# Kernel tuning notes

Measured on AMD Instinct MI355X. Metric: run time of the kernel, lower is better.

Reference implementation:

```python
import jax, jax.numpy as jnp
import numpy as np

B, T, D = 16, 4096, 1024
NUM_CLASSES = 1000
K, TOP_M = 4, 8
TEMP, EPS = 0.07, 1e-6


def setup_inputs() -> dict:
    key = jax.random.key(0)
    k_e, k_v, k_w = jax.random.split(key, 3)
    E = jax.random.normal(k_e, (B, T, D), dtype=jnp.float32)
    v = jax.random.normal(k_v, (K, D), dtype=jnp.float32) * 0.02
    m_logits = jnp.zeros((K, D), dtype=jnp.float32)
    cls_W = jax.random.normal(k_w, (K, NUM_CLASSES, D), dtype=jnp.float32) * (1.0 / D ** 0.5)
    cls_b = jnp.zeros((K, NUM_CLASSES), dtype=jnp.float32)
    beta = jnp.ones((K,), dtype=jnp.float32)
    alpha = jnp.ones((K,), dtype=jnp.float32)
    return {"E": E, "v": v, "m_logits": m_logits, "cls_W": cls_W,
            "cls_b": cls_b, "beta": beta, "alpha": alpha}


def reference(E, v, m_logits, cls_W, cls_b, beta, alpha):
    tokens = E  # (B, T, D)
    logits_sum = jnp.zeros((E.shape[0], cls_W.shape[1]), dtype=E.dtype)
    top_m = min(TOP_M, E.shape[1])
    for k in range(K):
        # unit peel direction u_k
        vk = v[k] * jax.nn.sigmoid(m_logits[k])          # (D,)
        u = vk / (jnp.linalg.norm(vk) + EPS)             # (D,)
        # token scores and soft attention
        coeff_all = jnp.einsum('btd,d->bt', tokens, u)   # (B, T) = E @ u
        scores = coeff_all / TEMP
        att = jax.nn.softmax(scores, axis=1)             # (B, T)
        # hard top-m tokens
        _, top_idx = jax.lax.top_k(scores, top_m)        # (B, m)
        top_tokens = jnp.take_along_axis(tokens, top_idx[:, :, None], axis=1)  # (B, m, D)
        # rank-1 projections onto u: proj(X) = (X@u)[...,None]*u
        coeff_top = jnp.einsum('bmd,d->bm', top_tokens, u)
        z_hard = jnp.sum(coeff_top, axis=1)[:, None] * u           # (B, D)
        z_soft = jnp.sum(coeff_all * att, axis=1)[:, None] * u     # (B, D)
        z_k = 0.5 * (z_hard + z_soft)
        logits_k = z_k @ cls_W[k].T + cls_b[k]                      # (B, C)
        logits_sum = logits_sum + alpha[k] * logits_k
        # residual peel: remove u component from all tokens
        tokens = tokens - beta[k] * (coeff_all[:, :, None] * u)
    return logits_sum
```

## Files before the change

kernel.cpp:

```cpp
#include <hip/hip_runtime.h>
#include <math.h>

#define DD 1024
#define TT 4096
#define BB 16
#define KK 4
#define CC 1000
#define TEMP_F 0.07f
#define EPS_F 1e-6f
#define NPROJ 2048

#define CE(a, b) { float _mx = fmaxf(a, b), _mn = fminf(a, b); a = _mx; b = _mn; }
#define INS8(y_) { float y = (y_); \
    CE(s0, y) CE(s1, y) CE(s2, y) CE(s3, y) CE(s4, y) CE(s5, y) CE(s6, y) CE(s7, y) }
#define RESORT8() { \
    CE(s0, s4) CE(s1, s5) CE(s2, s6) CE(s3, s7) \
    CE(s0, s2) CE(s1, s3) CE(s4, s6) CE(s5, s7) \
    CE(s0, s1) CE(s2, s3) CE(s4, s5) CE(s6, s7) }
#define WMERGE(off) { \
    float t0 = __shfl_xor(s0, off), t1 = __shfl_xor(s1, off), \
          t2 = __shfl_xor(s2, off), t3 = __shfl_xor(s3, off), \
          t4 = __shfl_xor(s4, off), t5 = __shfl_xor(s5, off), \
          t6 = __shfl_xor(s6, off), t7 = __shfl_xor(s7, off); \
    s0 = fmaxf(s0, t7); s1 = fmaxf(s1, t6); s2 = fmaxf(s2, t5); s3 = fmaxf(s3, t4); \
    s4 = fmaxf(s4, t3); s5 = fmaxf(s5, t2); s6 = fmaxf(s6, t1); s7 = fmaxf(s7, t0); \
    RESORT8() }
#define LMERGE(L) { \
    s0 = fmaxf(s0, (L)[7]); s1 = fmaxf(s1, (L)[6]); s2 = fmaxf(s2, (L)[5]); \
    s3 = fmaxf(s3, (L)[4]); s4 = fmaxf(s4, (L)[3]); s5 = fmaxf(s5, (L)[2]); \
    s6 = fmaxf(s6, (L)[1]); s7 = fmaxf(s7, (L)[0]); \
    RESORT8() }

__global__ __launch_bounds__(256) void k_u_g(const float* __restrict__ v,
                                             const float* __restrict__ m,
                                             float* __restrict__ u_ws,
                                             float* __restrict__ G_ws) {
    __shared__ float u_lds[KK * DD];
    int tid = threadIdx.x, w = tid >> 6, lane = tid & 63;
    float s_reg[16];
    float ss = 0.f;
#pragma unroll
    for (int i = 0; i < 16; ++i) {
        int d = lane + i * 64;
        float mv = m[w * DD + d];
        float s = v[w * DD + d] * (1.f / (1.f + expf(-mv)));
        s_reg[i] = s; ss += s * s;
    }
#pragma unroll
    for (int off = 32; off; off >>= 1) ss += __shfl_xor(ss, off);
    float inv = 1.f / (sqrtf(ss) + EPS_F);
#pragma unroll
    for (int i = 0; i < 16; ++i) {
        int d = lane + i * 64;
        float uu = s_reg[i] * inv;
        u_lds[w * DD + d] = uu;
        u_ws[w * DD + d] = uu;
    }
    __syncthreads();
    for (int p = w; p < 6; p += 4) {
        int j = (p < 3) ? 0 : ((p < 5) ? 1 : 2);
        int k = (p < 3) ? (p + 1) : ((p < 5) ? (p - 1) : 3);
        float acc = 0.f;
#pragma unroll
        for (int i = 0; i < 16; ++i) {
            int d = lane + i * 64;
            acc += u_lds[j * DD + d] * u_lds[k * DD + d];
        }
#pragma unroll
        for (int off = 32; off; off >>= 1) acc += __shfl_xor(acc, off);
        if (lane == 0) G_ws[j * KK + k] = acc;
    }
}

__global__ __launch_bounds__(256) void k_proj_wu(const float* __restrict__ E,
                                                 const float* __restrict__ W,
                                                 const float* __restrict__ u_ws,
                                                 float* __restrict__ c0,
                                                 float* __restrict__ wdot) {
    int tid = threadIdx.x, w = tid >> 6, lane = tid & 63;
    if (blockIdx.x < NPROJ) {
        float4 U[KK][4];
#pragma unroll
        for (int k = 0; k < KK; ++k)
#pragma unroll
            for (int j = 0; j < 4; ++j)
                U[k][j] = *reinterpret_cast<const float4*>(u_ws + k * DD + lane * 4 + j * 256);
        const int ITERS = (BB * TT) / (NPROJ * 4);
#pragma unroll 1
        for (int it = 0; it < ITERS; ++it) {
            size_t g = (size_t)(blockIdx.x * 4 + w) + (size_t)it * (NPROJ * 4);
            const float* e = E + g * DD;
            float a0 = 0.f, a1 = 0.f, a2 = 0.f, a3 = 0.f;
#pragma unroll
            for (int j = 0; j < 4; ++j) {
                float4 ev = *reinterpret_cast<const float4*>(e + lane * 4 + j * 256);
                a0 += ev.x * U[0][j].x + ev.y * U[0][j].y + ev.z * U[0][j].z + ev.w * U[0][j].w;
                a1 += ev.x * U[1][j].x + ev.y * U[1][j].y + ev.z * U[1][j].z + ev.w * U[1][j].w;
                a2 += ev.x * U[2][j].x + ev.y * U[2][j].y + ev.z * U[2][j].z + ev.w * U[2][j].w;
                a3 += ev.x * U[3][j].x + ev.y * U[3][j].y + ev.z * U[3][j].z + ev.w * U[3][j].w;
            }
#pragma unroll
            for (int off = 32; off; off >>= 1) {
                a0 += __shfl_xor(a0, off);
                a1 += __shfl_xor(a1, off);
                a2 += __shfl_xor(a2, off);
                a3 += __shfl_xor(a3, off);
            }
            if (lane == 0)
                *reinterpret_cast<float4*>(c0 + g * 4) = make_float4(a0, a1, a2, a3);
        }
    } else {
        int c = blockIdx.x - NPROJ;
        const float* wr = W + ((size_t)w * CC + c) * DD;
        const float* ur = u_ws + w * DD;
        float acc = 0.f;
#pragma unroll
        for (int j = 0; j < 4; ++j) {
            float4 wv = *reinterpret_cast<const float4*>(wr + lane * 4 + j * 256);
            float4 uv = *reinterpret_cast<const float4*>(ur + lane * 4 + j * 256);
            acc += wv.x * uv.x + wv.y * uv.y + wv.z * uv.z + wv.w * uv.w;
        }
#pragma unroll
        for (int off = 32; off; off >>= 1) acc += __shfl_xor(acc, off);
        if (lane == 0) wdot[w * CC + c] = acc;
    }
}

__global__ __launch_bounds__(256) void k_peel2(const float* __restrict__ c0,
                                               const float* __restrict__ G_ws,
                                               const float* __restrict__ beta,
                                               float* __restrict__ cscal) {
    __shared__ float redm[4], reds[4], redc[4];
    __shared__ float topl[4][8];
    int tid = threadIdx.x, w = tid >> 6, lane = tid & 63;
    int b = blockIdx.x >> 2, k = blockIdx.x & 3;
    float g01 = G_ws[0 * KK + 1], g02 = G_ws[0 * KK + 2], g03 = G_ws[0 * KK + 3];
    float g12 = G_ws[1 * KK + 2], g13 = G_ws[1 * KK + 3], g23 = G_ws[2 * KK + 3];
    float b0 = beta[0], b1 = beta[1], b2 = beta[2];
    float fk[16];
    float mx = -INFINITY;
#pragma unroll
    for (int i = 0; i < 16; ++i) {
        int t = tid + i * 256;
        float4 cv = *reinterpret_cast<const float4*>(c0 + ((size_t)b * TT + t) * 4);
        float f0 = cv.x;
        float f1 = cv.y - b0 * g01 * f0;
        float f2 = cv.z - b0 * g02 * f0 - b1 * g12 * f1;
        float f3 = cv.w - b0 * g03 * f0 - b1 * g13 * f1 - b2 * g23 * f2;
        float f = (k == 0) ? f0 : ((k == 1) ? f1 : ((k == 2) ? f2 : f3));
        fk[i] = f; mx = fmaxf(mx, f);
    }
#pragma unroll
    for (int off = 32; off; off >>= 1) mx = fmaxf(mx, __shfl_xor(mx, off));
    if (lane == 0) redm[w] = mx;
    __syncthreads();
    mx = fmaxf(fmaxf(redm[0], redm[1]), fmaxf(redm[2], redm[3]));
    const float invT = 1.f / TEMP_F;
    float se = 0.f, sce = 0.f;
#pragma unroll
    for (int i = 0; i < 16; ++i) {
        float e = expf((fk[i] - mx) * invT);
        se += e; sce += fk[i] * e;
    }
#pragma unroll
    for (int off = 32; off; off >>= 1) {
        se += __shfl_xor(se, off);
        sce += __shfl_xor(sce, off);
    }
    if (lane == 0) { reds[w] = se; redc[w] = sce; }
    __syncthreads();
    se = reds[0] + reds[1] + reds[2] + reds[3];
    sce = redc[0] + redc[1] + redc[2] + redc[3];
    float zsoft = sce / se;
    float s0 = -INFINITY, s1 = -INFINITY, s2 = -INFINITY, s3 = -INFINITY,
          s4 = -INFINITY, s5 = -INFINITY, s6 = -INFINITY, s7 = -INFINITY;
#pragma unroll
    for (int i = 0; i < 16; ++i) INS8(fk[i]);
    WMERGE(1) WMERGE(2) WMERGE(4) WMERGE(8) WMERGE(16) WMERGE(32)
    if (lane == 0) {
        topl[w][0] = s0; topl[w][1] = s1; topl[w][2] = s2; topl[w][3] = s3;
        topl[w][4] = s4; topl[w][5] = s5; topl[w][6] = s6; topl[w][7] = s7;
    }
    __syncthreads();
    if (tid == 0) {
        LMERGE(topl[1]) LMERGE(topl[2]) LMERGE(topl[3])
        float sumtop = s0 + s1 + s2 + s3 + s4 + s5 + s6 + s7;
        cscal[b * KK + k] = 0.5f * (sumtop + zsoft);
    }
}

__global__ __launch_bounds__(256) void k_out(const float* __restrict__ wdot,
                                             const float* __restrict__ bias,
                                             const float* __restrict__ alpha,
                                             const float* __restrict__ cscal,
                                             float* __restrict__ out) {
    int idx = blockIdx.x * 256 + threadIdx.x;
    if (idx >= BB * CC) return;
    int b = idx / CC, c = idx % CC;
    float s = 0.f;
#pragma unroll
    for (int k = 0; k < KK; ++k)
        s += alpha[k] * (cscal[b * KK + k] * wdot[k * CC + c] + bias[k * CC + c]);
    out[idx] = s;
}

extern "C" void kernel_launch(void* const* d_in, const int* in_sizes, int n_in,
                              void* d_out, int out_size, void* d_ws, size_t ws_size,
                              hipStream_t stream) {
    const float* E     = (const float*)d_in[0];
    const float* v     = (const float*)d_in[1];
    const float* m     = (const float*)d_in[2];
    const float* W     = (const float*)d_in[3];
    const float* cb    = (const float*)d_in[4];
    const float* beta  = (const float*)d_in[5];
    const float* alpha = (const float*)d_in[6];
    float* out = (float*)d_out;
    float* ws = (float*)d_ws;

    float* u_ws  = ws;
    float* G_ws  = ws + 4096;
    float* cscal = ws + 4112;
    float* wdot  = ws + 4176;
    float* c0    = ws + 8176;

    k_u_g<<<1, 256, 0, stream>>>(v, m, u_ws, G_ws);
    k_proj_wu<<<NPROJ + CC, 256, 0, stream>>>(E, W, u_ws, c0, wdot);
    k_peel2<<<BB * KK, 256, 0, stream>>>(c0, G_ws, beta, cscal);
    k_out<<<(BB * CC + 255) / 256, 256, 0, stream>>>(wdot, cb, alpha, cscal, out);
}
```

Baseline: 64.87 us.

## Fuse u/Gram setup into projection kernel and peel into output kernel

After: 72.13 us. 1.11x slower.

```diff
diff --git a/kernel.cpp b/kernel.cpp
--- a/kernel.cpp
+++ b/kernel.cpp
@@ -25,36 +25,33 @@
     s0 = fmaxf(s0, t7); s1 = fmaxf(s1, t6); s2 = fmaxf(s2, t5); s3 = fmaxf(s3, t4); \
     s4 = fmaxf(s4, t3); s5 = fmaxf(s5, t2); s6 = fmaxf(s6, t1); s7 = fmaxf(s7, t0); \
     RESORT8() }
-#define LMERGE(L) { \
-    s0 = fmaxf(s0, (L)[7]); s1 = fmaxf(s1, (L)[6]); s2 = fmaxf(s2, (L)[5]); \
-    s3 = fmaxf(s3, (L)[4]); s4 = fmaxf(s4, (L)[3]); s5 = fmaxf(s5, (L)[2]); \
-    s6 = fmaxf(s6, (L)[1]); s7 = fmaxf(s7, (L)[0]); \
-    RESORT8() }
 
-__global__ __launch_bounds__(256) void k_u_g(const float* __restrict__ v,
-                                             const float* __restrict__ m,
-                                             float* __restrict__ u_ws,
-                                             float* __restrict__ G_ws) {
+__global__ __launch_bounds__(256) void k_main(const float* __restrict__ E,
+                                              const float* __restrict__ W,
+                                              const float* __restrict__ v,
+                                              const float* __restrict__ m,
+                                              const float* __restrict__ beta,
+                                              float* __restrict__ c0,
+                                              float* __restrict__ wdot) {
     __shared__ float u_lds[KK * DD];
+    __shared__ float G_lds[6];
     int tid = threadIdx.x, w = tid >> 6, lane = tid & 63;
-    float s_reg[16];
-    float ss = 0.f;
+
+    {
+        float s_reg[16];
+        float ss = 0.f;
 #pragma unroll
-    for (int i = 0; i < 16; ++i) {
-        int d = lane + i * 64;
-        float mv = m[w * DD + d];
-        float s = v[w * DD + d] * (1.f / (1.f + expf(-mv)));
-        s_reg[i] = s; ss += s * s;
-    }
+        for (int i = 0; i < 16; ++i) {
+            int d = lane + i * 64;
+            float mv = m[w * DD + d];
+            float s = v[w * DD + d] * (1.f / (1.f + expf(-mv)));
+            s_reg[i] = s; ss += s * s;
+        }
 #pragma unroll
-    for (int off = 32; off; off >>= 1) ss += __shfl_xor(ss, off);
-    float inv = 1.f / (sqrtf(ss) + EPS_F);
+        for (int off = 32; off; off >>= 1) ss += __shfl_xor(ss, off);
+        float inv = 1.f / (sqrtf(ss) + EPS_F);
 #pragma unroll
-    for (int i = 0; i < 16; ++i) {
-        int d = lane + i * 64;
-        float uu = s_reg[i] * inv;
-        u_lds[w * DD + d] = uu;
-        u_ws[w * DD + d] = uu;
+        for (int i = 0; i < 16; ++i) u_lds[w * DD + lane + i * 64] = s_reg[i] * inv;
     }
     __syncthreads();
     for (int p = w; p < 6; p += 4) {
@@ -68,23 +65,20 @@
         }
 #pragma unroll
         for (int off = 32; off; off >>= 1) acc += __shfl_xor(acc, off);
-        if (lane == 0) G_ws[j * KK + k] = acc;
+        if (lane == 0) G_lds[p] = acc;
     }
-}
+    __syncthreads();
 
-__global__ __launch_bounds__(256) void k_proj_wu(const float* __restrict__ E,
-                                                 const float* __restrict__ W,
-                                                 const float* __restrict__ u_ws,
-                                                 float* __restrict__ c0,
-                                                 float* __restrict__ wdot) {
-    int tid = threadIdx.x, w = tid >> 6, lane = tid & 63;
     if (blockIdx.x < NPROJ) {
+        float g01 = G_lds[0], g02 = G_lds[1], g03 = G_lds[2];
+        float g12 = G_lds[3], g13 = G_lds[4], g23 = G_lds[5];
+        float b0 = beta[0], b1 = beta[1], b2 = beta[2];
         float4 U[KK][4];
 #pragma unroll
         for (int k = 0; k < KK; ++k)
 #pragma unroll
             for (int j = 0; j < 4; ++j)
-                U[k][j] = *reinterpret_cast<const float4*>(u_ws + k * DD + lane * 4 + j * 256);
+                U[k][j] = *reinterpret_cast<const float4*>(u_lds + k * DD + lane * 4 + j * 256);
         const int ITERS = (BB * TT) / (NPROJ * 4);
 #pragma unroll 1
         for (int it = 0; it < ITERS; ++it) {
@@ -106,18 +100,21 @@
                 a2 += __shfl_xor(a2, off);
                 a3 += __shfl_xor(a3, off);
             }
+            float f0 = a0;
+            float f1 = a1 - b0 * g01 * f0;
+            float f2 = a2 - b0 * g02 * f0 - b1 * g12 * f1;
+            float f3 = a3 - b0 * g03 * f0 - b1 * g13 * f1 - b2 * g23 * f2;
             if (lane == 0)
-                *reinterpret_cast<float4*>(c0 + g * 4) = make_float4(a0, a1, a2, a3);
+                *reinterpret_cast<float4*>(c0 + g * 4) = make_float4(f0, f1, f2, f3);
         }
     } else {
         int c = blockIdx.x - NPROJ;
         const float* wr = W + ((size_t)w * CC + c) * DD;
-        const float* ur = u_ws + w * DD;
         float acc = 0.f;
 #pragma unroll
         for (int j = 0; j < 4; ++j) {
             float4 wv = *reinterpret_cast<const float4*>(wr + lane * 4 + j * 256);
-            float4 uv = *reinterpret_cast<const float4*>(ur + lane * 4 + j * 256);
+            float4 uv = *reinterpret_cast<const float4*>(u_lds + w * DD + lane * 4 + j * 256);
             acc += wv.x * uv.x + wv.y * uv.y + wv.z * uv.z + wv.w * uv.w;
         }
 #pragma unroll
@@ -126,39 +123,29 @@
     }
 }
 
-__global__ __launch_bounds__(256) void k_peel2(const float* __restrict__ c0,
-                                               const float* __restrict__ G_ws,
-                                               const float* __restrict__ beta,
-                                               float* __restrict__ cscal) {
-    __shared__ float redm[4], reds[4], redc[4];
-    __shared__ float topl[4][8];
+__global__ __launch_bounds__(256) void k_peel_out(const float* __restrict__ c0,
+                                                  const float* __restrict__ wdot,
+                                                  const float* __restrict__ bias,
+                                                  const float* __restrict__ alpha,
+                                                  float* __restrict__ out) {
+    __shared__ float csc[KK];
     int tid = threadIdx.x, w = tid >> 6, lane = tid & 63;
-    int b = blockIdx.x >> 2, k = blockIdx.x & 3;
-    float g01 = G_ws[0 * KK + 1], g02 = G_ws[0 * KK + 2], g03 = G_ws[0 * KK + 3];
-    float g12 = G_ws[1 * KK + 2], g13 = G_ws[1 * KK + 3], g23 = G_ws[2 * KK + 3];
-    float b0 = beta[0], b1 = beta[1], b2 = beta[2];
-    float fk[16];
+    int b = blockIdx.x;
+    float fk[64];
     float mx = -INFINITY;
 #pragma unroll
-    for (int i = 0; i < 16; ++i) {
-        int t = tid + i * 256;
+    for (int i = 0; i < 64; ++i) {
+        int t = lane + i * 64;
         float4 cv = *reinterpret_cast<const float4*>(c0 + ((size_t)b * TT + t) * 4);
-        float f0 = cv.x;
-        float f1 = cv.y - b0 * g01 * f0;
-        float f2 = cv.z - b0 * g02 * f0 - b1 * g12 * f1;
-        float f3 = cv.w - b0 * g03 * f0 - b1 * g13 * f1 - b2 * g23 * f2;
-        float f = (k == 0) ? f0 : ((k == 1) ? f1 : ((k == 2) ? f2 : f3));
+        float f = (w == 0) ? cv.x : ((w == 1) ? cv.y : ((w == 2) ? cv.z : cv.w));
         fk[i] = f; mx = fmaxf(mx, f);
     }
 #pragma unroll
     for (int off = 32; off; off >>= 1) mx = fmaxf(mx, __shfl_xor(mx, off));
-    if (lane == 0) redm[w] = mx;
-    __syncthreads();
-    mx = fmaxf(fmaxf(redm[0], redm[1]), fmaxf(redm[2], redm[3]));
     const float invT = 1.f / TEMP_F;
     float se = 0.f, sce = 0.f;
 #pragma unroll
-    for (int i = 0; i < 16; ++i) {
+    for (int i = 0; i < 64; ++i) {
         float e = expf((fk[i] - mx) * invT);
         se += e; sce += fk[i] * e;
     }
@@ -167,41 +154,26 @@
         se += __shfl_xor(se, off);
         sce += __shfl_xor(sce, off);
     }
-    if (lane == 0) { reds[w] = se; redc[w] = sce; }
-    __syncthreads();
-    se = reds[0] + reds[1] + reds[2] + reds[3];
-    sce = redc[0] + redc[1] + redc[2] + redc[3];
     float zsoft = sce / se;
     float s0 = -INFINITY, s1 = -INFINITY, s2 = -INFINITY, s3 = -INFINITY,
           s4 = -INFINITY, s5 = -INFINITY, s6 = -INFINITY, s7 = -INFINITY;
 #pragma unroll
-    for (int i = 0; i < 16; ++i) INS8(fk[i]);
+    for (int i = 0; i < 64; ++i) INS8(fk[i]);
     WMERGE(1) WMERGE(2) WMERGE(4) WMERGE(8) WMERGE(16) WMERGE(32)
     if (lane == 0) {
-        topl[w][0] = s0; topl[w][1] = s1; topl[w][2] = s2; topl[w][3] = s3;
-        topl[w][4] = s4; topl[w][5] = s5; topl[w][6] = s6; topl[w][7] = s7;
+        float sumtop = s0 + s1 + s2 + s3 + s4 + s5 + s6 + s7;
+        csc[w] = 0.5f * (sumtop + zsoft);
     }
     __syncthreads();
-    if (tid == 0) {
-        LMERGE(topl[1]) LMERGE(topl[2]) LMERGE(topl[3])
-        float sumtop = s0 + s1 + s2 + s3 + s4 + s5 + s6 + s7;
-        cscal[b * KK + k] = 0.5f * (sumtop + zsoft);
+    float al0 = alpha[0], al1 = alpha[1], al2 = alpha[2], al3 = alpha[3];
+    float c0s = csc[0], c1s = csc[1], c2s = csc[2], c3s = csc[3];
+    for (int c = tid; c < CC; c += 256) {
+        float s = al0 * (c0s * wdot[0 * CC + c] + bias[0 * CC + c])
+                + al1 * (c1s * wdot[1 * CC + c] + bias[1 * CC + c])
+                + al2 * (c2s * wdot[2 * CC + c] + bias[2 * CC + c])
+                + al3 * (c3s * wdot[3 * CC + c] + bias[3 * CC + c]);
+        out[(size_t)b * CC + c] = s;
     }
-}
-
-__global__ __launch_bounds__(256) void k_out(const float* __restrict__ wdot,
-                                             const float* __restrict__ bias,
-                                             const float* __restrict__ alpha,
-                                             const float* __restrict__ cscal,
-                                             float* __restrict__ out) {
-    int idx = blockIdx.x * 256 + threadIdx.x;
-    if (idx >= BB * CC) return;
-    int b = idx / CC, c = idx % CC;
-    float s = 0.f;
-#pragma unroll
-    for (int k = 0; k < KK; ++k)
-        s += alpha[k] * (cscal[b * KK + k] * wdot[k * CC + c] + bias[k * CC + c]);
-    out[idx] = s;
 }
 
 extern "C" void kernel_launch(void* const* d_in, const int* in_sizes, int n_in,
@@ -217,14 +189,9 @@
     float* out = (float*)d_out;
     float* ws = (float*)d_ws;
 
-    float* u_ws  = ws;
-    float* G_ws  = ws + 4096;
-    float* cscal = ws + 4112;
-    float* wdot  = ws + 4176;
-    float* c0    = ws + 8176;
+    float* wdot = ws;
+    float* c0   = ws + 4096;
 
-    k_u_g<<<1, 256, 0, stream>>>(v, m, u_ws, G_ws);
-    k_proj_wu<<<NPROJ + CC, 256, 0, stream>>>(E, W, u_ws, c0, wdot);
-    k_peel2<<<BB * KK, 256, 0, stream>>>(c0, G_ws, beta, cscal);
-    k_out<<<(BB * CC + 255) / 256, 256, 0, stream>>>(wdot, cb, alpha, cscal, out);
+    k_main<<<NPROJ + CC, 256, 0, stream>>>(E, W, v, m, beta, c0, wdot);
+    k_peel_out<<<BB, 256, 0, stream>>>(c0, wdot, cb, alpha, out);
 }
```
